# Performance work log

Measured on AMD Instinct MI355X. Metric: run time of the kernel, lower is better.

Reference implementation:

```python
import jax, jax.numpy as jnp
import numpy as np

B, N, C = 4, 32768, 128
L, H = 16, 8
D = C // H
NB = N // L
EG_H = 16  # EDGE_GATE_HIDDEN_DIM


def setup_inputs() -> dict:
    key = jax.random.key(0)
    ks = jax.random.split(key, 16)
    inp = {}
    inp["x"] = jax.random.normal(ks[0], (B, N, C), dtype=jnp.float32)
    inp["attn_mask"] = jax.random.randint(ks[1], (B, NB, L, L), 0, 2, dtype=jnp.int32)
    inp["edge_feats"] = jax.random.normal(ks[2], (B, NB, L, L, 4), dtype=jnp.float32)
    # learned parameters
    inp["Wqkv"] = jax.random.normal(ks[3], (3 * C, C), dtype=jnp.float32) * (C ** -0.5)
    inp["bqkv"] = jnp.zeros((3 * C,), dtype=jnp.float32)
    inp["Wproj"] = jax.random.normal(ks[4], (C, C), dtype=jnp.float32) * (C ** -0.5)
    inp["bproj"] = jnp.zeros((C,), dtype=jnp.float32)
    inp["eg_w1"] = jax.random.normal(ks[5], (EG_H, 4), dtype=jnp.float32) * 0.01
    inp["eg_b1"] = jnp.zeros((EG_H,), dtype=jnp.float32)
    inp["eg_w2"] = jax.random.normal(ks[6], (H, EG_H), dtype=jnp.float32) * 0.01
    inp["eg_b2"] = jnp.zeros((H,), dtype=jnp.float32)
    inp["Wbr"] = jax.random.normal(ks[7], (H, C), dtype=jnp.float32) * 0.01
    inp["bbr"] = jnp.zeros((H,), dtype=jnp.float32)
    return inp


def reference(x, attn_mask, edge_feats, Wqkv, bqkv, Wproj, bproj,
              eg_w1, eg_b1, eg_w2, eg_b2, Wbr, bbr):
    scale = D ** -0.5
    xb = x.reshape(B, NB, L, C)
    idx = jnp.arange(L)

    # bias_physics: zero the diagonal, set channel-3 diagonal to 1
    bp = edge_feats.at[:, :, idx, idx, :].set(0.0)
    bp = bp.at[:, :, idx, idx, 3].set(1.0)

    # mask: force diagonal on for rows with no valid key
    m = attn_mask.astype(x.dtype)
    need = (m.sum(axis=-1) < 1).astype(x.dtype)            # (B,NB,L)
    m = m.at[:, :, idx, idx].set(jnp.maximum(m[:, :, idx, idx], need))

    # qkv per block
    qkv = xb @ Wqkv.T + bqkv                               # (B,NB,L,3C)
    q = qkv[..., :C].reshape(B, NB, L, H, D)
    k = qkv[..., C:2 * C].reshape(B, NB, L, H, D)
    v = qkv[..., 2 * C:].reshape(B, NB, L, H, D)

    # edge-gate MLP -> per-head linear edge weights (zeroed where masked)
    h1 = jax.nn.gelu(bp @ eg_w1.T + eg_b1, approximate=False)
    ew = h1 @ eg_w2.T + eg_b2                              # (B,NB,L,L,H)
    ew = jnp.where(m[..., None] == 0, 0.0, ew)

    # logit bias = physics channel 3, masked with -inf
    logit = jnp.where(m == 0, -jnp.inf, bp[..., 3])        # (B,NB,L,L)

    scores = jnp.einsum('bnqhd,bnkhd->bnhqk', q, k) * scale + logit[:, :, None]
    attn = jax.nn.softmax(scores, axis=-1)
    x_soft = jnp.einsum('bnhqk,bnkhd->bnqhd', attn, v)

    # linear edge-weight mixing of values
    x_mid = x_soft + jnp.einsum('bnqkh,bnkhd->bnqhd', ew, v)

    # block node (use_block_node=True): mean token per block, gated value add
    blk = xb.mean(axis=2, keepdims=True)                   # (B,NB,1,C)
    v_blk = (blk @ Wqkv.T + bqkv)[..., 2 * C:].reshape(B, NB, 1, H, D)
    g_blk = jax.nn.sigmoid(xb @ Wbr.T + bbr)               # (B,NB,L,H)
    x_mid = x_mid + g_blk[..., None] * v_blk

    out = x_mid.reshape(B, N, C) @ Wproj.T + bproj
    return out
```

## Files before the change

kernel.cpp:

```cpp
#include <hip/hip_runtime.h>
#include <hip/hip_bf16.h>
#include <math.h>

typedef __attribute__((ext_vector_type(8))) short bf16x8;
typedef __attribute__((ext_vector_type(4))) short bf16x4;
typedef __attribute__((ext_vector_type(4))) float f32x4;
typedef __attribute__((ext_vector_type(4))) unsigned short us4;

#define NITER 8

static __device__ __forceinline__ unsigned short f2bf_rn(float f) {
    union { __hip_bfloat16 h; unsigned short u; } cv;
    cv.h = __float2bfloat16(f);
    return cv.u;
}
static __device__ __forceinline__ float bf2f(unsigned short u) {
    union { unsigned int i; float f; } cv;
    cv.i = ((unsigned int)u) << 16;
    return cv.f;
}
static __device__ __forceinline__ f32x4 MFMA(bf16x8 a, bf16x8 b, f32x4 c) {
    return __builtin_amdgcn_mfma_f32_16x16x32_bf16(a, b, c, 0, 0, 0);
}
static __device__ __forceinline__ f32x4 MFMA16(bf16x4 a, bf16x4 b, f32x4 c) {
#if __has_builtin(__builtin_amdgcn_mfma_f32_16x16x16bf16_1k)
    return __builtin_amdgcn_mfma_f32_16x16x16bf16_1k(a, b, c, 0, 0, 0);
#elif __has_builtin(__builtin_amdgcn_mfma_f32_16x16x16_bf16)
    return __builtin_amdgcn_mfma_f32_16x16x16_bf16(a, b, c, 0, 0, 0);
#else
    f32x4 d;
    asm("v_mfma_f32_16x16x16_bf16 %0, %1, %2, %3"
        : "=v"(d) : "v"(a), "v"(b), "v"(c));
    return d;
#endif
}
static __device__ __forceinline__ float sigmoid_fast(float t) {
    return __builtin_amdgcn_rcpf(1.f + __expf(-t));
}

__global__ __launch_bounds__(256) void prep_kernel(
    const float* __restrict__ Wqkv, const float* __restrict__ Wbr,
    const float* __restrict__ Wproj,
    unsigned short* __restrict__ Wbig, unsigned short* __restrict__ Wp)
{
    int i = blockIdx.x * 256 + threadIdx.x;
    if (i < 400 * 128) {
        int n = i >> 7, k = i & 127;
        float v = (n < 384) ? Wqkv[i] : (n < 392 ? Wbr[(n - 384) * 128 + k] : 0.f);
        Wbig[i] = f2bf_rn(v);
    } else {
        int j = i - 400 * 128;
        if (j < 128 * 128) Wp[j] = f2bf_rn(Wproj[j]);
    }
}

__global__ __launch_bounds__(512) void leaf_main(
    const float* __restrict__ x, const int* __restrict__ mask,
    const float* __restrict__ edge,
    const unsigned short* __restrict__ Wbig, const unsigned short* __restrict__ Wp,
    const float* __restrict__ bqkv, const float* __restrict__ bproj,
    const float* __restrict__ eg_w1, const float* __restrict__ eg_b1,
    const float* __restrict__ eg_w2, const float* __restrict__ eg_b2,
    const float* __restrict__ bbr, float* __restrict__ out)
{
    __shared__ unsigned short xS[16 * 128];
    __shared__ unsigned short mhiS[16 * 136];
    __shared__ unsigned short ewS[8 * 256];
    __shared__ float logitS[256];
    __shared__ float mlpW1[16 * 4];
    __shared__ float mlpB1[16];
    __shared__ float mlpW2T[16 * 8];

    const int tid  = threadIdx.x;
    const int lane = tid & 63;
    const int wave = tid >> 6;
    const int c15  = lane & 15;
    const int quad = lane >> 4;
    const int bid0 = blockIdx.x * NITER;

    const f32x4 bqv = *(const f32x4*)&bqkv[wave * 16 + quad * 4];
    const f32x4 bkv = *(const f32x4*)&bqkv[128 + wave * 16 + quad * 4];
    const float bq2 = bqkv[256 + wave * 16 + c15];
    const float bgate = bbr[c15 & 7];
    const float bpv = bproj[wave * 16 + c15];

    if (tid < 16) {
        const int j = tid;
        #pragma unroll
        for (int i = 0; i < 4; ++i) mlpW1[j * 4 + i] = eg_w1[j * 4 + i];
        mlpB1[j] = eg_b1[j];
        #pragma unroll
        for (int h = 0; h < 8; ++h) mlpW2T[j * 8 + h] = eg_w2[h * 16 + j];
    }

    const unsigned short* wbase = Wbig + c15 * 128 + quad * 8;
    bf16x8 Bq[4], Bk[4], Bv[4], Wt[4];
    {
        const unsigned short* wq = wbase + (wave * 16) * 128;
        const unsigned short* wk = wbase + ((8 + wave) * 16) * 128;
        const unsigned short* wv = wbase + ((16 + wave) * 16) * 128;
        const unsigned short* wp = Wp + (wave * 16 + c15) * 128 + quad * 8;
        #pragma unroll
        for (int kk = 0; kk < 4; ++kk) {
            Bq[kk] = *(const bf16x8*)(wq + kk * 32);
            Bk[kk] = *(const bf16x8*)(wk + kk * 32);
            Bv[kk] = *(const bf16x8*)(wv + kk * 32);
            Wt[kk] = *(const bf16x8*)(wp + kk * 32);
        }
    }
    const unsigned short* wg = wbase + 384 * 128;

    int mv = 0;
    float4 evv = make_float4(0.f, 0.f, 0.f, 0.f);
    if (tid < 256) {
        mv  = mask[(size_t)bid0 * 256 + tid];
        evv = *(const float4*)&edge[((size_t)bid0 * 256 + tid) * 4];
    }
    float4 xv = ((const float4*)(x + (size_t)bid0 * 2048))[tid];
    {
        int row = tid >> 5, c4 = tid & 31;
        int off = row * 128 + (((c4 >> 1) ^ (row & 7)) << 3) + ((c4 & 1) << 2);
        us4 hi;
        hi[0] = f2bf_rn(xv.x); hi[1] = f2bf_rn(xv.y);
        hi[2] = f2bf_rn(xv.z); hi[3] = f2bf_rn(xv.w);
        *(us4*)&xS[off] = hi;
    }
    __syncthreads();

    #pragma unroll 1
    for (int it = 0; it < NITER; ++it) {
        const int bid = bid0 + it;
        const bool more = (it + 1 < NITER);

        bf16x8 Bg[4];
        #pragma unroll
        for (int kk = 0; kk < 4; ++kk) Bg[kk] = *(const bf16x8*)(wg + kk * 32);

        float4 xv_n = make_float4(0.f, 0.f, 0.f, 0.f);
        int mv_n = 0;
        float4 ev_n = make_float4(0.f, 0.f, 0.f, 0.f);
        if (more) {
            xv_n = ((const float4*)(x + (size_t)(bid + 1) * 2048))[tid];
            if (tid < 256) {
                mv_n = mask[(size_t)(bid + 1) * 256 + tid];
                ev_n = *(const float4*)&edge[((size_t)(bid + 1) * 256 + tid) * 4];
            }
        }

        if (tid < 256) {
            const int q = tid >> 4, k = tid & 15;
            unsigned long long b = __ballot(mv != 0);
            int rs = __popcll((b >> (lane & 48)) & 0xFFFFull);
            float m = (float)mv;
            if (q == k && rs < 1) m = 1.f;
            float bp0, bp1, bp2, bp3;
            if (q == k) { bp0 = bp1 = bp2 = 0.f; bp3 = 1.f; }
            else        { bp0 = evv.x; bp1 = evv.y; bp2 = evv.z; bp3 = evv.w; }
            logitS[tid] = (m == 0.f) ? -INFINITY : bp3;
            float ew[8];
            #pragma unroll
            for (int h = 0; h < 8; ++h) ew[h] = eg_b2[h];
            #pragma unroll
            for (int j = 0; j < 16; ++j) {
                const f32x4 w1j = *(const f32x4*)&mlpW1[j * 4];
                float z = __builtin_fmaf(w1j[0], bp0,
                          __builtin_fmaf(w1j[1], bp1,
                          __builtin_fmaf(w1j[2], bp2,
                          __builtin_fmaf(w1j[3], bp3, mlpB1[j]))));
                float u = z * z;
                float w = __builtin_fmaf(-0.0664904f, u, 0.3989423f);
                float g = z * __builtin_fmaf(z, w, 0.5f);
                const f32x4 wa = *(const f32x4*)&mlpW2T[j * 8];
                const f32x4 wb = *(const f32x4*)&mlpW2T[j * 8 + 4];
                ew[0] = __builtin_fmaf(wa[0], g, ew[0]);
                ew[1] = __builtin_fmaf(wa[1], g, ew[1]);
                ew[2] = __builtin_fmaf(wa[2], g, ew[2]);
                ew[3] = __builtin_fmaf(wa[3], g, ew[3]);
                ew[4] = __builtin_fmaf(wb[0], g, ew[4]);
                ew[5] = __builtin_fmaf(wb[1], g, ew[5]);
                ew[6] = __builtin_fmaf(wb[2], g, ew[6]);
                ew[7] = __builtin_fmaf(wb[3], g, ew[7]);
            }
            #pragma unroll
            for (int h = 0; h < 8; ++h)
                ewS[h * 256 + tid] = (m == 0.f) ? (unsigned short)0
                                   : (unsigned short)(__float_as_uint(ew[h]) >> 16);
        }

        bf16x8 ah[4];
        #pragma unroll
        for (int kk = 0; kk < 4; ++kk) {
            int off = c15 * 128 + (((kk * 4 + quad) ^ (c15 & 7)) << 3);
            ah[kk] = *(const bf16x8*)&xS[off];
        }

        bf16x4 qa, ka, va;
        float vblk;
        float greg[4];

        {
            f32x4 acc = {0.f, 0.f, 0.f, 0.f};
            #pragma unroll
            for (int kk = 0; kk < 4; ++kk) acc = MFMA(Bq[kk], ah[kk], acc);
            #pragma unroll
            for (int r = 0; r < 4; ++r) qa[r] = (short)f2bf_rn(acc[r] + bqv[r]);
        }

        {
            f32x4 acc = {0.f, 0.f, 0.f, 0.f};
            #pragma unroll
            for (int kk = 0; kk < 4; ++kk) acc = MFMA(Bk[kk], ah[kk], acc);
            #pragma unroll
            for (int r = 0; r < 4; ++r) ka[r] = (short)f2bf_rn(acc[r] + bkv[r]);
        }

        {
            f32x4 acc = {0.f, 0.f, 0.f, 0.f};
            #pragma unroll
            for (int kk = 0; kk < 4; ++kk) acc = MFMA(ah[kk], Bv[kk], acc);
            #pragma unroll
            for (int r = 0; r < 4; ++r) va[r] = (short)f2bf_rn(acc[r] + bq2);
            float s = acc[0] + acc[1] + acc[2] + acc[3];
            s += __shfl_xor(s, 16);
            s += __shfl_xor(s, 32);
            vblk = s * 0.0625f + bq2;
        }

        {
            f32x4 acc = {0.f, 0.f, 0.f, 0.f};
            #pragma unroll
            for (int kk = 0; kk < 4; ++kk) acc = MFMA(ah[kk], Bg[kk], acc);
            const int src = (lane & 48) | wave;
            #pragma unroll
            for (int r = 0; r < 4; ++r) {
                float sg = sigmoid_fast(acc[r] + bgate);
                greg[r] = __shfl(sg, src);
            }
        }
        __syncthreads();

        if (more) {
            int row = tid >> 5, c4 = tid & 31;
            int off = row * 128 + (((c4 >> 1) ^ (row & 7)) << 3) + ((c4 & 1) << 2);
            us4 hi;
            hi[0] = f2bf_rn(xv_n.x); hi[1] = f2bf_rn(xv_n.y);
            hi[2] = f2bf_rn(xv_n.z); hi[3] = f2bf_rn(xv_n.w);
            *(us4*)&xS[off] = hi;
        }

        {
            f32x4 sc = {0.f, 0.f, 0.f, 0.f};
            sc = MFMA16(ka, qa, sc);
            const f32x4 lg = *(const f32x4*)&logitS[c15 * 16 + quad * 4];
            const us4 ew4 = *(const us4*)&ewS[wave * 256 + c15 * 16 + quad * 4];
            float e0 = __expf(__builtin_fmaf(sc[0], 0.25f, lg[0]));
            float e1 = __expf(__builtin_fmaf(sc[1], 0.25f, lg[1]));
            float e2 = __expf(__builtin_fmaf(sc[2], 0.25f, lg[2]));
            float e3 = __expf(__builtin_fmaf(sc[3], 0.25f, lg[3]));
            float sm = (e0 + e1) + (e2 + e3);
            sm += __shfl_xor(sm, 16);
            sm += __shfl_xor(sm, 32);
            const float inv = __builtin_amdgcn_rcpf(sm);
            bf16x4 pa;
            pa[0] = (short)f2bf_rn(__builtin_fmaf(e0, inv, bf2f(ew4[0])));
            pa[1] = (short)f2bf_rn(__builtin_fmaf(e1, inv, bf2f(ew4[1])));
            pa[2] = (short)f2bf_rn(__builtin_fmaf(e2, inv, bf2f(ew4[2])));
            pa[3] = (short)f2bf_rn(__builtin_fmaf(e3, inv, bf2f(ew4[3])));
            f32x4 xs = {0.f, 0.f, 0.f, 0.f};
            xs = MFMA16(pa, va, xs);
            #pragma unroll
            for (int r = 0; r < 4; ++r) {
                const int tok = quad * 4 + r;
                float val = xs[r] + greg[r] * vblk;
                mhiS[tok * 136 + wave * 16 + c15] = f2bf_rn(val);
            }
        }
        __syncthreads();

        {
            bf16x8 mh[4];
            #pragma unroll
            for (int kk = 0; kk < 4; ++kk)
                mh[kk] = *(const bf16x8*)&mhiS[c15 * 136 + kk * 32 + quad * 8];
            f32x4 acc = {0.f, 0.f, 0.f, 0.f};
            #pragma unroll
            for (int kk = 0; kk < 4; ++kk) acc = MFMA(mh[kk], Wt[kk], acc);
            float* op = out + (size_t)bid * 2048;
            #pragma unroll
            for (int r = 0; r < 4; ++r)
                op[(quad * 4 + r) * 128 + wave * 16 + c15] = acc[r] + bpv;
        }

        mv = mv_n;
        evv = ev_n;
    }
}

extern "C" void kernel_launch(void* const* d_in, const int* in_sizes, int n_in,
                              void* d_out, int out_size, void* d_ws, size_t ws_size,
                              hipStream_t stream) {
    const float* x     = (const float*)d_in[0];
    const int*   amask = (const int*)  d_in[1];
    const float* edge  = (const float*)d_in[2];
    const float* Wqkv  = (const float*)d_in[3];
    const float* bqkv  = (const float*)d_in[4];
    const float* Wproj = (const float*)d_in[5];
    const float* bproj = (const float*)d_in[6];
    const float* eg_w1 = (const float*)d_in[7];
    const float* eg_b1 = (const float*)d_in[8];
    const float* eg_w2 = (const float*)d_in[9];
    const float* eg_b2 = (const float*)d_in[10];
    const float* Wbr   = (const float*)d_in[11];
    const float* bbr   = (const float*)d_in[12];
    float* outp = (float*)d_out;

    unsigned short* Wbig = (unsigned short*)d_ws;
    unsigned short* Wp   = (unsigned short*)((char*)d_ws + 400 * 128 * 2);

    hipLaunchKernelGGL(prep_kernel, dim3(264), dim3(256), 0, stream,
                       Wqkv, Wbr, Wproj, Wbig, Wp);
    hipLaunchKernelGGL(leaf_main, dim3(8192 / NITER), dim3(512), 0, stream,
                       x, amask, edge, Wbig, Wp, bqkv, bproj,
                       eg_w1, eg_b1, eg_w2, eg_b2, bbr, outp);
}
```

Baseline: 96.11 us.

## Compute edge-gate MLP with small MFMAs spread across all waves

```diff
diff --git a/kernel.cpp b/kernel.cpp
--- a/kernel.cpp
+++ b/kernel.cpp
@@ -67,9 +67,6 @@
     __shared__ unsigned short mhiS[16 * 136];
     __shared__ unsigned short ewS[8 * 256];
     __shared__ float logitS[256];
-    __shared__ float mlpW1[16 * 4];
-    __shared__ float mlpB1[16];
-    __shared__ float mlpW2T[16 * 8];
 
     const int tid  = threadIdx.x;
     const int lane = tid & 63;
@@ -77,6 +74,7 @@
     const int c15  = lane & 15;
     const int quad = lane >> 4;
     const int bid0 = blockIdx.x * NITER;
+    const int t0 = wave * 2, t1 = wave * 2 + 1;
 
     const f32x4 bqv = *(const f32x4*)&bqkv[wave * 16 + quad * 4];
     const f32x4 bkv = *(const f32x4*)&bqkv[128 + wave * 16 + quad * 4];
@@ -84,14 +82,21 @@
     const float bgate = bbr[c15 & 7];
     const float bpv = bproj[wave * 16 + c15];
 
-    if (tid < 16) {
-        const int j = tid;
-        #pragma unroll
-        for (int i = 0; i < 4; ++i) mlpW1[j * 4 + i] = eg_w1[j * 4 + i];
-        mlpB1[j] = eg_b1[j];
-        #pragma unroll
-        for (int h = 0; h < 8; ++h) mlpW2T[j * 8 + h] = eg_w2[h * 16 + j];
-    }
+    bf16x4 W1a = {0, 0, 0, 0};
+    if (quad == 0) {
+        const f32x4 w1 = *(const f32x4*)&eg_w1[c15 * 4];
+        #pragma unroll
+        for (int r = 0; r < 4; ++r) W1a[r] = (short)f2bf_rn(w1[r]);
+    }
+    bf16x4 W2a = {0, 0, 0, 0};
+    if (c15 < 8) {
+        const f32x4 w2 = *(const f32x4*)&eg_w2[c15 * 16 + quad * 4];
+        #pragma unroll
+        for (int r = 0; r < 4; ++r) W2a[r] = (short)f2bf_rn(w2[r]);
+    }
+    const f32x4 b1v = *(const f32x4*)&eg_b1[quad * 4];
+    f32x4 b2v = {0.f, 0.f, 0.f, 0.f};
+    if (quad < 2) b2v = *(const f32x4*)&eg_b2[quad * 4];
 
     const unsigned short* wbase = Wbig + c15 * 128 + quad * 8;
     bf16x8 Bq[4], Bk[4], Bv[4], Wt[4];
@@ -110,11 +115,15 @@
     }
     const unsigned short* wg = wbase + 384 * 128;
 
-    int mv = 0;
-    float4 evv = make_float4(0.f, 0.f, 0.f, 0.f);
-    if (tid < 256) {
-        mv  = mask[(size_t)bid0 * 256 + tid];
-        evv = *(const float4*)&edge[((size_t)bid0 * 256 + tid) * 4];
+    int mvA = 0, mvB = 0;
+    float4 evA = make_float4(0.f, 0.f, 0.f, 0.f);
+    float4 evB = make_float4(0.f, 0.f, 0.f, 0.f);
+    if (quad == 0) {
+        const size_t base = (size_t)bid0 * 256;
+        mvA = mask[base + t0 * 16 + c15];
+        mvB = mask[base + t1 * 16 + c15];
+        evA = *(const float4*)&edge[(base + t0 * 16 + c15) * 4];
+        evB = *(const float4*)&edge[(base + t1 * 16 + c15) * 4];
     }
     float4 xv = ((const float4*)(x + (size_t)bid0 * 2048))[tid];
     {
@@ -137,54 +146,62 @@
         for (int kk = 0; kk < 4; ++kk) Bg[kk] = *(const bf16x8*)(wg + kk * 32);
 
         float4 xv_n = make_float4(0.f, 0.f, 0.f, 0.f);
-        int mv_n = 0;
-        float4 ev_n = make_float4(0.f, 0.f, 0.f, 0.f);
+        int mvA_n = 0, mvB_n = 0;
+        float4 evA_n = make_float4(0.f, 0.f, 0.f, 0.f);
+        float4 evB_n = make_float4(0.f, 0.f, 0.f, 0.f);
         if (more) {
             xv_n = ((const float4*)(x + (size_t)(bid + 1) * 2048))[tid];
-            if (tid < 256) {
-                mv_n = mask[(size_t)(bid + 1) * 256 + tid];
-                ev_n = *(const float4*)&edge[((size_t)(bid + 1) * 256 + tid) * 4];
-            }
-        }
-
-        if (tid < 256) {
-            const int q = tid >> 4, k = tid & 15;
-            unsigned long long b = __ballot(mv != 0);
-            int rs = __popcll((b >> (lane & 48)) & 0xFFFFull);
-            float m = (float)mv;
-            if (q == k && rs < 1) m = 1.f;
-            float bp0, bp1, bp2, bp3;
-            if (q == k) { bp0 = bp1 = bp2 = 0.f; bp3 = 1.f; }
-            else        { bp0 = evv.x; bp1 = evv.y; bp2 = evv.z; bp3 = evv.w; }
-            logitS[tid] = (m == 0.f) ? -INFINITY : bp3;
-            float ew[8];
-            #pragma unroll
-            for (int h = 0; h < 8; ++h) ew[h] = eg_b2[h];
-            #pragma unroll
-            for (int j = 0; j < 16; ++j) {
-                const f32x4 w1j = *(const f32x4*)&mlpW1[j * 4];
-                float z = __builtin_fmaf(w1j[0], bp0,
-                          __builtin_fmaf(w1j[1], bp1,
-                          __builtin_fmaf(w1j[2], bp2,
-                          __builtin_fmaf(w1j[3], bp3, mlpB1[j]))));
+            if (quad == 0) {
+                const size_t base = (size_t)(bid + 1) * 256;
+                mvA_n = mask[base + t0 * 16 + c15];
+                mvB_n = mask[base + t1 * 16 + c15];
+                evA_n = *(const float4*)&edge[(base + t0 * 16 + c15) * 4];
+                evB_n = *(const float4*)&edge[(base + t1 * 16 + c15) * 4];
+            }
+        }
+
+        #pragma unroll
+        for (int tt = 0; tt < 2; ++tt) {
+            const int t = tt ? t1 : t0;
+            const int mvt = tt ? mvB : mvA;
+            const float4 evt = tt ? evB : evA;
+            bf16x4 bpB = {0, 0, 0, 0};
+            float bp3 = 0.f;
+            if (quad == 0) {
+                const bool diag = (c15 == t);
+                bp3 = diag ? 1.f : evt.w;
+                bpB[0] = (short)f2bf_rn(diag ? 0.f : evt.x);
+                bpB[1] = (short)f2bf_rn(diag ? 0.f : evt.y);
+                bpB[2] = (short)f2bf_rn(diag ? 0.f : evt.z);
+                bpB[3] = (short)f2bf_rn(bp3);
+            }
+            const unsigned long long bl = __ballot(quad == 0 && mvt != 0);
+            const unsigned m16 = (unsigned)(bl & 0xFFFFull);
+            const bool meff = ((m16 >> c15) & 1u) || (m16 == 0u && c15 == t);
+            if (quad == 0)
+                logitS[t * 16 + c15] = meff ? bp3 : -INFINITY;
+            f32x4 h1 = {0.f, 0.f, 0.f, 0.f};
+            h1 = MFMA16(W1a, bpB, h1);
+            bf16x4 hB;
+            #pragma unroll
+            for (int r = 0; r < 4; ++r) {
+                float z = h1[r] + b1v[r];
                 float u = z * z;
                 float w = __builtin_fmaf(-0.0664904f, u, 0.3989423f);
                 float g = z * __builtin_fmaf(z, w, 0.5f);
-                const f32x4 wa = *(const f32x4*)&mlpW2T[j * 8];
-                const f32x4 wb = *(const f32x4*)&mlpW2T[j * 8 + 4];
-                ew[0] = __builtin_fmaf(wa[0], g, ew[0]);
-                ew[1] = __builtin_fmaf(wa[1], g, ew[1]);
-                ew[2] = __builtin_fmaf(wa[2], g, ew[2]);
-                ew[3] = __builtin_fmaf(wa[3], g, ew[3]);
-                ew[4] = __builtin_fmaf(wb[0], g, ew[4]);
-                ew[5] = __builtin_fmaf(wb[1], g, ew[5]);
-                ew[6] = __builtin_fmaf(wb[2], g, ew[6]);
-                ew[7] = __builtin_fmaf(wb[3], g, ew[7]);
-            }
-            #pragma unroll
-            for (int h = 0; h < 8; ++h)
-                ewS[h * 256 + tid] = (m == 0.f) ? (unsigned short)0
-                                   : (unsigned short)(__float_as_uint(ew[h]) >> 16);
+                hB[r] = (short)f2bf_rn(g);
+            }
+            f32x4 e2 = {0.f, 0.f, 0.f, 0.f};
+            e2 = MFMA16(W2a, hB, e2);
+            if (quad < 2) {
+                #pragma unroll
+                for (int r = 0; r < 4; ++r) {
+                    float ewv = e2[r] + b2v[r];
+                    ewS[(quad * 4 + r) * 256 + t * 16 + c15] =
+                        meff ? (unsigned short)(__float_as_uint(ewv) >> 16)
+                             : (unsigned short)0;
+                }
+            }
         }
 
         bf16x8 ah[4];
@@ -291,8 +308,8 @@
                 op[(quad * 4 + r) * 128 + wave * 16 + c15] = acc[r] + bpv;
         }
 
-        mv = mv_n;
-        evv = ev_n;
+        mvA = mvA_n; mvB = mvB_n;
+        evA = evA_n; evB = evB_n;
     }
 }
 
```

Result: faster. 85.43 us (-11.1%).
